# Kernel optimization log

Measured on AMD Instinct MI355X. Metric: run time of the kernel, lower is better.

## Reference

```python
import jax, jax.numpy as jnp
import numpy as np

B, T, C = 2, 2048, 1024
H = 4 * C           # MLP hidden (4*n_embd)
E_DYN = 7           # num_experts - static_experts
TOP_K = 2           # num_experts_per_tok
MOE_LOSS_COEF = 0.01


def setup_inputs() -> dict:
    key = jax.random.key(0)
    ks = jax.random.split(key, 6)
    s = 0.02
    x = jax.random.normal(ks[0], (B, T, C), dtype=jnp.float32)
    gate_w = jax.random.normal(ks[1], (C, E_DYN), dtype=jnp.float32) * s
    w1 = jax.random.normal(ks[2], (E_DYN, C, H), dtype=jnp.float32) * s   # dynamic experts c_fc
    w2 = jax.random.normal(ks[3], (E_DYN, H, C), dtype=jnp.float32) * s   # dynamic experts c_proj
    w1s = jax.random.normal(ks[4], (C, H), dtype=jnp.float32) * s         # static expert c_fc
    w2s = jax.random.normal(ks[5], (H, C), dtype=jnp.float32) * s         # static expert c_proj
    return {"x": x, "gate_w": gate_w, "w1": w1, "w2": w2, "w1s": w1s, "w2s": w2s}


def reference(x, gate_w, w1, w2, w1s, w2s):
    b, t, c = x.shape
    xf = x.reshape(-1, c)                                   # [N, C]
    n = xf.shape[0]

    # static expert (always applied)
    y_static = jax.nn.gelu(xf @ w1s, approximate=False) @ w2s  # [N, C]

    # gating: top-k + softmax over selected scores
    scores = xf @ gate_w                                    # [N, E]
    topk_scores, topk_idx = jax.lax.top_k(scores, TOP_K)    # [N, K]
    topk_w = jax.nn.softmax(topk_scores, axis=-1)           # [N, K]

    # dense dispatch weights [N, E] (top_k indices are distinct -> set is safe)
    probs = jnp.zeros((n, E_DYN), dtype=x.dtype)
    probs = probs.at[jnp.arange(n)[:, None], topk_idx].set(topk_w)

    # all-expert MLP then weighted combine (same math as masked per-expert dispatch)
    h = jax.nn.gelu(jnp.einsum('nc,ech->enh', xf, w1), approximate=False)  # [E, N, H]
    y_all = jnp.einsum('enh,ehc->enc', h, w2)               # [E, N, C]
    y_dyn = jnp.einsum('ne,enc->nc', probs, y_all)          # [N, C]

    y = (y_dyn + y_static).reshape(b, t, c)

    # variance_penalty auxiliary loss
    expert_usage = probs.mean(axis=0)                       # [E]
    variance = jnp.mean((expert_usage - expert_usage.mean()) ** 2)
    aux = MOE_LOSS_COEF * variance
    return y, aux
```

## Files before the change

kernel.cpp:

```cpp
#include <hip/hip_runtime.h>
#include <hip/hip_bf16.h>
#include <math.h>

#define N_TOK 4096
#define C_DIM 1024
#define H_DIM 4096
#define NEXP 7
#define NGRP 8
#define HCAP 13184

typedef __attribute__((ext_vector_type(8))) short short8;
typedef __attribute__((ext_vector_type(4))) float floatx4;

static const size_t OFF_COUNTS = 0;
static const size_t OFF_CURSOR = 64;
static const size_t OFF_BASE   = 128;
static const size_t OFF_PCOUNT = 192;
static const size_t OFF_CNT8   = 256;
static const size_t OFF_USAGE  = 320;
static const size_t OFF_TOPKI  = 4096;
static const size_t OFF_TOPKW  = OFF_TOPKI + 8192ull * 4;
static const size_t OFF_ETOK   = OFF_TOPKW + 8192ull * 4;
static const size_t OFF_EWT    = OFF_ETOK + (size_t)HCAP * 4;
static const size_t OFF_EIDX   = OFF_EWT + (size_t)HCAP * 4;
static const size_t OFF_XB     = 262144;
static const size_t OFF_W1T    = OFF_XB + (size_t)N_TOK * C_DIM * 2;
static const size_t OFF_W2T    = OFF_W1T + (size_t)NGRP * H_DIM * C_DIM * 2;
static const size_t OFF_H      = OFF_W2T + (size_t)NGRP * C_DIM * H_DIM * 2;

static __device__ __forceinline__ unsigned short f2bf(float f) {
    __hip_bfloat16 b = __float2bfloat16(f);
    return *reinterpret_cast<unsigned short*>(&b);
}
static __device__ __forceinline__ float bf2f(unsigned short u) {
    unsigned int v = ((unsigned int)u) << 16;
    return __builtin_bit_cast(float, v);
}

static __device__ __forceinline__ float gelu_f(float v) {
    float z = v * 0.70710678118654752f;
    float az = fabsf(z);
    float t = 1.0f / (1.0f + 0.3275911f * az);
    float poly = t * (0.254829592f + t * (-0.284496736f + t * (1.421413741f +
                 t * (-1.453152027f + t * 1.061405429f))));
    float erf_abs = 1.0f - poly * __expf(-az * az);
    float erf_v = (z < 0.f) ? -erf_abs : erf_abs;
    return 0.5f * v * (1.0f + erf_v);
}

static __device__ __forceinline__ void gll16(const void* g, void* l) {
    __builtin_amdgcn_global_load_lds((const __attribute__((address_space(1))) void*)g,
                                     (__attribute__((address_space(3))) void*)l, 16, 0, 0);
}

static __device__ __forceinline__ void barf() {
    __builtin_amdgcn_s_barrier();
    asm volatile("" ::: "memory");
}
#define LGKM0 asm volatile("s_waitcnt lgkmcnt(0)" ::: "memory")
#define VMC6  asm volatile("s_waitcnt vmcnt(6)" ::: "memory")
#define VMC0  asm volatile("s_waitcnt vmcnt(0)" ::: "memory")
#define PRIO1 __builtin_amdgcn_s_setprio(1)
#define PRIO0 __builtin_amdgcn_s_setprio(0)

__global__ void init_small_kernel(int* counts, int* cursor, float* usage) {
    int i = threadIdx.x;
    if (i < 8) { counts[i] = 0; cursor[i] = 0; usage[i] = 0.f; }
}

__global__ __launch_bounds__(256) void transpose_cvt_kernel(
    const float* __restrict__ w1, const float* __restrict__ w1s,
    const float* __restrict__ w2, const float* __restrict__ w2s,
    __hip_bfloat16* __restrict__ w1t, __hip_bfloat16* __restrict__ w2t)
{
    int bid = blockIdx.x;
    int fam = bid >> 13;
    int r = bid & 8191;
    int e = r >> 10;
    int t_ = r & 1023;
    int R, S, s0, r0;
    const float* src; unsigned short* d;
    if (fam == 0) {
        R = C_DIM; S = H_DIM;
        src = (e < NEXP) ? (w1 + (size_t)e * R * S) : w1s;
        d = (unsigned short*)(w1t) + (size_t)e * R * S;
        s0 = (t_ & 63) * 64; r0 = (t_ >> 6) * 64;
    } else {
        R = H_DIM; S = C_DIM;
        src = (e < NEXP) ? (w2 + (size_t)e * R * S) : w2s;
        d = (unsigned short*)(w2t) + (size_t)e * R * S;
        s0 = (t_ & 15) * 64; r0 = (t_ >> 4) * 64;
    }
    __shared__ float t[64][65];
    int lx = (threadIdx.x & 15) * 4, ty = threadIdx.x >> 4;
#pragma unroll
    for (int i = 0; i < 4; i++) {
        int rr = ty + i * 16;
        float4 v = *(const float4*)(src + (size_t)(r0 + rr) * S + s0 + lx);
        t[rr][lx] = v.x; t[rr][lx + 1] = v.y; t[rr][lx + 2] = v.z; t[rr][lx + 3] = v.w;
    }
    __syncthreads();
#pragma unroll
    for (int i = 0; i < 4; i++) {
        int ss = ty + i * 16;
        ushort4 o;
        o.x = f2bf(t[lx][ss]); o.y = f2bf(t[lx + 1][ss]);
        o.z = f2bf(t[lx + 2][ss]); o.w = f2bf(t[lx + 3][ss]);
        *(ushort4*)(d + (size_t)(s0 + ss) * R + r0 + lx) = o;
    }
}

__global__ __launch_bounds__(256) void gate_kernel(
    const float* __restrict__ x, const float* __restrict__ gw,
    unsigned short* __restrict__ xb,
    int* __restrict__ topki, float* __restrict__ topkw,
    int* counts, float* usage)
{
    int wid = threadIdx.x >> 6, lane = threadIdx.x & 63;
    int t = blockIdx.x * 4 + wid;
    float s[NEXP];
#pragma unroll
    for (int e = 0; e < NEXP; e++) s[e] = 0.f;
#pragma unroll
    for (int it = 0; it < 4; ++it) {
        int c = it * 256 + lane * 4;
        float4 xv = *(const float4*)(x + (size_t)t * C_DIM + c);
        ushort4 o;
        o.x = f2bf(xv.x); o.y = f2bf(xv.y); o.z = f2bf(xv.z); o.w = f2bf(xv.w);
        *(ushort4*)(xb + (size_t)t * C_DIM + c) = o;
        const float* g0 = gw + (size_t)c * NEXP;
#pragma unroll
        for (int e = 0; e < NEXP; e++) s[e] += xv.x * g0[e];
#pragma unroll
        for (int e = 0; e < NEXP; e++) s[e] += xv.y * g0[NEXP + e];
#pragma unroll
        for (int e = 0; e < NEXP; e++) s[e] += xv.z * g0[2 * NEXP + e];
#pragma unroll
        for (int e = 0; e < NEXP; e++) s[e] += xv.w * g0[3 * NEXP + e];
    }
#pragma unroll
    for (int e = 0; e < NEXP; e++)
        for (int off = 32; off > 0; off >>= 1) s[e] += __shfl_xor(s[e], off);
    if (lane == 0) {
        int e0 = 0;
        for (int e = 1; e < NEXP; e++) if (s[e] > s[e0]) e0 = e;
        int e1 = -1;
        for (int e = 0; e < NEXP; e++) {
            if (e == e0) continue;
            if (e1 < 0 || s[e] > s[e1]) e1 = e;
        }
        float w0 = 1.f / (1.f + expf(s[e1] - s[e0]));
        float w1 = 1.f - w0;
        topki[t * 2] = e0; topki[t * 2 + 1] = e1;
        topkw[t * 2] = w0; topkw[t * 2 + 1] = w1;
        atomicAdd(&counts[e0], 1); atomicAdd(&counts[e1], 1);
        atomicAdd(&usage[e0], w0); atomicAdd(&usage[e1], w1);
    }
}

__global__ __launch_bounds__(256) void prefix_kernel(
    const int* counts, const float* usage,
    int* base, int* pcount, int* cnt8,
    int* etok, float* ewt, float* y, int aux_index)
{
    __shared__ int sb[NGRP], sc[NGRP], sp[NGRP];
    if (threadIdx.x == 0) {
        int run = 0;
        for (int g = 0; g < NEXP; g++) {
            int c = counts[g];
            int p = (c + 127) & ~127;
            base[g] = run; pcount[g] = p; cnt8[g] = c;
            sb[g] = run; sc[g] = c; sp[g] = p;
            run += p;
        }
        base[NEXP] = run; pcount[NEXP] = N_TOK; cnt8[NEXP] = N_TOK;
        sb[NEXP] = run; sc[NEXP] = N_TOK; sp[NEXP] = N_TOK;
        float u[NEXP]; float mean = 0.f;
        for (int e = 0; e < NEXP; e++) { u[e] = usage[e] / (float)N_TOK; mean += u[e]; }
        mean /= (float)NEXP;
        float var = 0.f;
        for (int e = 0; e < NEXP; e++) { float dd = u[e] - mean; var += dd * dd; }
        var /= (float)NEXP;
        y[aux_index] = 0.01f * var;
    }
    __syncthreads();
    for (int i = threadIdx.x; i < N_TOK; i += 256) {
        etok[sb[NEXP] + i] = i; ewt[sb[NEXP] + i] = 1.0f;
    }
    for (int g = 0; g < NEXP; g++) {
        for (int i = sc[g] + (int)threadIdx.x; i < sp[g]; i += 256) {
            etok[sb[g] + i] = 0; ewt[sb[g] + i] = 0.f;
        }
    }
}

__global__ void scatter_kernel(const int* __restrict__ topki, const float* __restrict__ topkw,
                               const int* __restrict__ base, int* cursor,
                               int* __restrict__ etok, float* __restrict__ ewt,
                               int* __restrict__ eidx)
{
    int i = blockIdx.x * 256 + threadIdx.x;
    int t = i >> 1;
    int e = topki[i];
    float w = topkw[i];
    int pos = atomicAdd(&cursor[e], 1);
    int idx = base[e] + pos;
    etok[idx] = t; ewt[idx] = w;
    eidx[i] = idx;
}


static __device__ __forceinline__ void mfma16(const short8 (&a)[8], const short8 (&b)[4],
                                              floatx4 (&acc)[8][4], int mo, int no) {
#pragma unroll
    for (int i = 0; i < 4; i++)
#pragma unroll
        for (int j = 0; j < 2; j++)
#pragma unroll
            for (int kk = 0; kk < 2; kk++)
                acc[mo + i][no + j] = __builtin_amdgcn_mfma_f32_16x16x32_bf16(
                    a[i * 2 + kk], b[j * 2 + kk], acc[mo + i][no + j], 0, 0, 0);
}
static __device__ __forceinline__ void rdA(short8 (&d)[8], const char* b, int sw0, int sw1) {
#pragma unroll
    for (int i = 0; i < 4; i++) {
        d[i * 2]     = *(const short8*)(b + i * 2048 + sw0);
        d[i * 2 + 1] = *(const short8*)(b + i * 2048 + sw1);
    }
}
static __device__ __forceinline__ void rdB(short8 (&d)[4], const char* b, int sw0, int sw1) {
#pragma unroll
    for (int j = 0; j < 2; j++) {
        d[j * 2]     = *(const short8*)(b + j * 2048 + sw0);
        d[j * 2 + 1] = *(const short8*)(b + j * 2048 + sw1);
    }
}

static __device__ __forceinline__ void gemm_core(char* lds, int NKT,
    const char* pA0, const char* pA1, const char* pA2, const char* pA3,
    const char* pB0, const char* pB1, const char* pB2, const char* pB3,
    floatx4 (&acc)[8][4])
{
    int tid = threadIdx.x, lane = tid & 63, w = tid >> 6;
    int wm = w >> 2, wn = w & 3, l16 = lane & 15, quad = lane >> 4;
    int sw0 = ((quad ^ (l16 & 7)) << 4);
    int sw1 = (((4 + quad) ^ (l16 & 7)) << 4);
    int aoff = (wm * 64 + l16) * 128;
    int boff = (wn * 32 + l16) * 128;
    int wb = w * 1024;
    short8 aM0[8], aM1[8], bN0[4], bN1[4];

#define SA_(h, doff, ko) do { \
    gll16(((h) ? pA1 : pA0) + (ko), lds + (doff) + (h) * 16384 + wb); \
    gll16(((h) ? pA3 : pA2) + (ko), lds + (doff) + (h) * 16384 + 8192 + wb); } while (0)
#define SB_(nh, doff, ko) do { \
    gll16(((nh) ? pB1 : pB0) + (ko), lds + 65536 + (doff) + (nh) * 16384 + wb); \
    gll16(((nh) ? pB3 : pB2) + (ko), lds + 65536 + (doff) + (nh) * 16384 + 8192 + wb); } while (0)

    SA_(0, 0, 0); SA_(1, 0, 0); SB_(0, 0, 0); SB_(1, 0, 0);
    SA_(0, 32768, 128); SA_(1, 32768, 128); SB_(0, 32768, 128);
    VMC6;
    barf();

#pragma unroll 1
    for (int T = 0; T < NKT - 2; ++T) {
        int curo = (T & 1) << 15;
        int nxto = curo ^ 32768;
        rdB(bN0, lds + 65536 + curo + boff, sw0, sw1);
        rdA(aM0, lds + curo + aoff, sw0, sw1);
        SB_(1, nxto, 128);
        barf();
        PRIO1; mfma16(aM0, bN0, acc, 0, 0); PRIO0;
        LGKM0; barf();
        rdA(aM1, lds + curo + 16384 + aoff, sw0, sw1);
        SA_(0, curo, 256);
        barf();
        PRIO1; mfma16(aM1, bN0, acc, 4, 0); PRIO0;
        LGKM0; barf();
        rdB(bN1, lds + 65536 + curo + 16384 + boff, sw0, sw1);
        SA_(1, curo, 256);
        barf();
        PRIO1; mfma16(aM0, bN1, acc, 0, 2); PRIO0;
        LGKM0; barf();
        SB_(0, curo, 256);
        barf();
        PRIO1; mfma16(aM1, bN1, acc, 4, 2); PRIO0;
        VMC6;
        barf();
        pA0 += 128; pA1 += 128; pA2 += 128; pA3 += 128;
        pB0 += 128; pB1 += 128; pB2 += 128; pB3 += 128;
    }
    {
        int curo = ((NKT - 2) & 1) << 15;
        int nxto = curo ^ 32768;
        rdB(bN0, lds + 65536 + curo + boff, sw0, sw1);
        rdA(aM0, lds + curo + aoff, sw0, sw1);
        SB_(1, nxto, 128);
        barf();
        PRIO1; mfma16(aM0, bN0, acc, 0, 0); PRIO0;
        LGKM0; barf();
        rdA(aM1, lds + curo + 16384 + aoff, sw0, sw1);
        barf();
        PRIO1; mfma16(aM1, bN0, acc, 4, 0); PRIO0;
        LGKM0; barf();
        rdB(bN1, lds + 65536 + curo + 16384 + boff, sw0, sw1);
        barf();
        PRIO1; mfma16(aM0, bN1, acc, 0, 2); PRIO0;
        LGKM0; barf();
        PRIO1; mfma16(aM1, bN1, acc, 4, 2); PRIO0;
        VMC0;
        barf();
        int lasto = nxto;
        rdB(bN0, lds + 65536 + lasto + boff, sw0, sw1);
        rdA(aM0, lds + lasto + aoff, sw0, sw1);
        rdA(aM1, lds + lasto + 16384 + aoff, sw0, sw1);
        rdB(bN1, lds + 65536 + lasto + 16384 + boff, sw0, sw1);
        mfma16(aM0, bN0, acc, 0, 0);
        mfma16(aM1, bN0, acc, 4, 0);
        mfma16(aM0, bN1, acc, 0, 2);
        mfma16(aM1, bN1, acc, 4, 2);
    }
#undef SA_
#undef SB_
}

__global__ __launch_bounds__(512, 2) void gemm1_kernel(
    const __hip_bfloat16* __restrict__ xb,
    const __hip_bfloat16* __restrict__ w1t,
    __hip_bfloat16* __restrict__ h,
    const int* __restrict__ etok,
    const int* __restrict__ base,
    const int* __restrict__ pcount)
{
    int id = blockIdx.x;
    int xcd = id & 7, rest = id >> 3;
    int ct = rest & 15, s = rest >> 4;
    int g = s & 7;
    int mt = ((xcd - g) & 7) + 8 * (s >> 3);
    int psz = pcount[g];
    if (mt * 256 >= psz) return;
    int eb = base[g];

    __shared__ __align__(16) char lds[131072];

    int tid = threadIdx.x, lane = tid & 63, w = tid >> 6;
    int u0 = 8 * w + (lane >> 3);
    int v  = (u0 & 31) + ((u0 >> 5) << 6);
    int ssw = ((lane & 7) ^ (lane >> 3)) * 16;

    int t0 = etok[eb + mt * 256 + u0];
    int t1 = etok[eb + mt * 256 + 64 + u0];
    int t2 = etok[eb + mt * 256 + 128 + u0];
    int t3 = etok[eb + mt * 256 + 192 + u0];
    const char* pA0 = (const char*)(xb + (size_t)t0 * C_DIM) + ssw;
    const char* pA1 = (const char*)(xb + (size_t)t1 * C_DIM) + ssw;
    const char* pA2 = (const char*)(xb + (size_t)t2 * C_DIM) + ssw;
    const char* pA3 = (const char*)(xb + (size_t)t3 * C_DIM) + ssw;
    const char* pB0 = (const char*)(w1t + ((size_t)g * H_DIM + ct * 256 + v) * C_DIM) + ssw;
    const char* pB1 = (const char*)(w1t + ((size_t)g * H_DIM + ct * 256 + v + 32) * C_DIM) + ssw;
    const char* pB2 = (const char*)(w1t + ((size_t)g * H_DIM + ct * 256 + v + 128) * C_DIM) + ssw;
    const char* pB3 = (const char*)(w1t + ((size_t)g * H_DIM + ct * 256 + v + 160) * C_DIM) + ssw;

    floatx4 acc[8][4] = {};
    gemm_core(lds, C_DIM / 64, pA0, pA1, pA2, pA3, pB0, pB1, pB2, pB3, acc);

    int wm = w >> 2, wn = w & 3, l16 = lane & 15, quad = lane >> 4;
#pragma unroll
    for (int i = 0; i < 8; i++) {
        int lr0 = mt * 256 + wm * 128 + i * 16 + quad * 4;
#pragma unroll
        for (int reg = 0; reg < 4; reg++) {
            int lr = lr0 + reg;
            if (lr < psz) {
                size_t hrow = (size_t)(eb + lr) * H_DIM;
#pragma unroll
                for (int j = 0; j < 4; j++) {
                    int cc = ct * 256 + wn * 64 + j * 16 + l16;
                    h[hrow + cc] = __float2bfloat16(gelu_f(acc[i][j][reg]));
                }
            }
        }
    }
}

__global__ __launch_bounds__(512, 2) void gemm2_kernel(
    const __hip_bfloat16* __restrict__ h,
    const __hip_bfloat16* __restrict__ w2t,
    unsigned short* __restrict__ yp,
    const int* __restrict__ base,
    const int* __restrict__ pcount)
{
    int id = blockIdx.x;
    int xcd = id & 7, rest = id >> 3;
    int ct = rest & 3, s = rest >> 2;
    int g = s & 7;
    int mt = ((xcd - g) & 7) + 8 * (s >> 3);
    int psz = pcount[g];
    if (mt * 256 >= psz) return;
    int eb = base[g];

    __shared__ __align__(16) char lds[131072];

    int tid = threadIdx.x, lane = tid & 63, w = tid >> 6;
    int u0 = 8 * w + (lane >> 3);
    int v  = (u0 & 31) + ((u0 >> 5) << 6);
    int ssw = ((lane & 7) ^ (lane >> 3)) * 16;

    const char* pA0 = (const char*)(h + (size_t)(eb + mt * 256 + u0) * H_DIM) + ssw;
    const char* pA1 = (const char*)(h + (size_t)(eb + mt * 256 + 64 + u0) * H_DIM) + ssw;
    const char* pA2 = (const char*)(h + (size_t)(eb + mt * 256 + 128 + u0) * H_DIM) + ssw;
    const char* pA3 = (const char*)(h + (size_t)(eb + mt * 256 + 192 + u0) * H_DIM) + ssw;
    const char* pB0 = (const char*)(w2t + ((size_t)g * C_DIM + ct * 256 + v) * H_DIM) + ssw;
    const char* pB1 = (const char*)(w2t + ((size_t)g * C_DIM + ct * 256 + v + 32) * H_DIM) + ssw;
    const char* pB2 = (const char*)(w2t + ((size_t)g * C_DIM + ct * 256 + v + 128) * H_DIM) + ssw;
    const char* pB3 = (const char*)(w2t + ((size_t)g * C_DIM + ct * 256 + v + 160) * H_DIM) + ssw;

    floatx4 acc[8][4] = {};
    gemm_core(lds, H_DIM / 64, pA0, pA1, pA2, pA3, pB0, pB1, pB2, pB3, acc);

    int wm = w >> 2, wn = w & 3, l16 = lane & 15, quad = lane >> 4;
#pragma unroll
    for (int i = 0; i < 8; i++) {
        int lr0 = mt * 256 + wm * 128 + i * 16 + quad * 4;
#pragma unroll
        for (int reg = 0; reg < 4; reg++) {
            int lr = lr0 + reg;
            if (lr < psz) {
                size_t yrow = (size_t)(eb + lr) * C_DIM;
#pragma unroll
                for (int j = 0; j < 4; j++) {
                    int cc = ct * 256 + wn * 64 + j * 16 + l16;
                    yp[yrow + cc] = f2bf(acc[i][j][reg]);
                }
            }
        }
    }
}

__global__ __launch_bounds__(256) void combine_kernel(
    const unsigned short* __restrict__ yp,
    const int* __restrict__ eidx,
    const float* __restrict__ topkw,
    const int* __restrict__ base,
    float* __restrict__ y)
{
    int t = blockIdx.x;
    int i0 = eidx[t * 2], i1 = eidx[t * 2 + 1];
    float w0 = topkw[t * 2], w1 = topkw[t * 2 + 1];
    int is = base[NEXP] + t;
    int c = threadIdx.x * 4;
    ushort4 a = *(const ushort4*)(yp + (size_t)i0 * C_DIM + c);
    ushort4 b = *(const ushort4*)(yp + (size_t)i1 * C_DIM + c);
    ushort4 s = *(const ushort4*)(yp + (size_t)is * C_DIM + c);
    float4 o;
    o.x = w0 * bf2f(a.x) + w1 * bf2f(b.x) + bf2f(s.x);
    o.y = w0 * bf2f(a.y) + w1 * bf2f(b.y) + bf2f(s.y);
    o.z = w0 * bf2f(a.z) + w1 * bf2f(b.z) + bf2f(s.z);
    o.w = w0 * bf2f(a.w) + w1 * bf2f(b.w) + bf2f(s.w);
    *(float4*)(y + (size_t)t * C_DIM + c) = o;
}

extern "C" void kernel_launch(void* const* d_in, const int* in_sizes, int n_in,
                              void* d_out, int out_size, void* d_ws, size_t ws_size,
                              hipStream_t stream) {
    const float* x      = (const float*)d_in[0];
    const float* gate_w = (const float*)d_in[1];
    const float* w1     = (const float*)d_in[2];
    const float* w2     = (const float*)d_in[3];
    const float* w1s    = (const float*)d_in[4];
    const float* w2s    = (const float*)d_in[5];
    float* y = (float*)d_out;
    char* ws = (char*)d_ws;

    int*   counts = (int*)(ws + OFF_COUNTS);
    int*   cursor = (int*)(ws + OFF_CURSOR);
    int*   base   = (int*)(ws + OFF_BASE);
    int*   pcount = (int*)(ws + OFF_PCOUNT);
    int*   cnt8   = (int*)(ws + OFF_CNT8);
    float* usage  = (float*)(ws + OFF_USAGE);
    int*   topki  = (int*)(ws + OFF_TOPKI);
    float* topkw  = (float*)(ws + OFF_TOPKW);
    int*   etok   = (int*)(ws + OFF_ETOK);
    float* ewt    = (float*)(ws + OFF_EWT);
    int*   eidx   = (int*)(ws + OFF_EIDX);
    unsigned short* xb_u = (unsigned short*)(ws + OFF_XB);
    __hip_bfloat16* xb  = (__hip_bfloat16*)(ws + OFF_XB);
    __hip_bfloat16* w1t = (__hip_bfloat16*)(ws + OFF_W1T);
    __hip_bfloat16* w2t = (__hip_bfloat16*)(ws + OFF_W2T);
    __hip_bfloat16* hbuf = (__hip_bfloat16*)(ws + OFF_H);
    unsigned short* yp  = (unsigned short*)(ws + OFF_W1T);

    init_small_kernel<<<1, 64, 0, stream>>>(counts, cursor, usage);

    transpose_cvt_kernel<<<16384, 256, 0, stream>>>(w1, w1s, w2, w2s, w1t, w2t);

    gate_kernel<<<N_TOK / 4, 256, 0, stream>>>(x, gate_w, xb_u, topki, topkw, counts, usage);
    prefix_kernel<<<1, 256, 0, stream>>>(counts, usage, base, pcount, cnt8, etok, ewt, y, N_TOK * C_DIM);
    scatter_kernel<<<(N_TOK * 2) / 256, 256, 0, stream>>>(topki, topkw, base, cursor, etok, ewt, eidx);

    gemm1_kernel<<<4096, 512, 0, stream>>>(xb, w1t, hbuf, etok, base, pcount);
    gemm2_kernel<<<1024, 512, 0, stream>>>(hbuf, w2t, yp, base, pcount);
    combine_kernel<<<N_TOK, 256, 0, stream>>>(yp, eidx, topkw, base, y);
}
```

Baseline: 712.2 us.

## Restructure GEMM core pipeline to prefetch LDS fragments ahead of MFMAs

Reworks the shared GEMM main loop so LDS fragment reads for the next sub-tile are issued before the current MFMA batch, dropping the explicit lgkmcnt(0) waits. The loop is unrolled by two with compile-time buffer offsets, and K-tile counts and B strides become template parameters so the four B pointers collapse into one base plus constant offsets, freeing registers. The MFMA loop order is changed to iterate k outermost, and the occupancy hint of 2 blocks per CU is removed from launch_bounds. Overlapping LDS reads with MFMAs needs more live fragment registers and relies on the compiler inserting correct waits.

```diff
diff --git a/kernel.cpp b/kernel.cpp
--- a/kernel.cpp
+++ b/kernel.cpp
@@ -57,8 +57,7 @@
     __builtin_amdgcn_s_barrier();
     asm volatile("" ::: "memory");
 }
-#define LGKM0 asm volatile("s_waitcnt lgkmcnt(0)" ::: "memory")
-#define VMC6  asm volatile("s_waitcnt vmcnt(6)" ::: "memory")
+#define VMC2  asm volatile("s_waitcnt vmcnt(2)" ::: "memory")
 #define VMC0  asm volatile("s_waitcnt vmcnt(0)" ::: "memory")
 #define PRIO1 __builtin_amdgcn_s_setprio(1)
 #define PRIO0 __builtin_amdgcn_s_setprio(0)
@@ -213,11 +212,11 @@
 static __device__ __forceinline__ void mfma16(const short8 (&a)[8], const short8 (&b)[4],
                                               floatx4 (&acc)[8][4], int mo, int no) {
 #pragma unroll
-    for (int i = 0; i < 4; i++)
-#pragma unroll
-        for (int j = 0; j < 2; j++)
-#pragma unroll
-            for (int kk = 0; kk < 2; kk++)
+    for (int kk = 0; kk < 2; kk++)
+#pragma unroll
+        for (int i = 0; i < 4; i++)
+#pragma unroll
+            for (int j = 0; j < 2; j++)
                 acc[mo + i][no + j] = __builtin_amdgcn_mfma_f32_16x16x32_bf16(
                     a[i * 2 + kk], b[j * 2 + kk], acc[mo + i][no + j], 0, 0, 0);
 }
@@ -236,10 +235,10 @@
     }
 }
 
-static __device__ __forceinline__ void gemm_core(char* lds, int NKT,
+template <int NKT, size_t KB>
+static __device__ __forceinline__ void gemm_core(char* lds,
     const char* pA0, const char* pA1, const char* pA2, const char* pA3,
-    const char* pB0, const char* pB1, const char* pB2, const char* pB3,
-    floatx4 (&acc)[8][4])
+    const char* pB0, floatx4 (&acc)[8][4])
 {
     int tid = threadIdx.x, lane = tid & 63, w = tid >> 6;
     int wm = w >> 2, wn = w & 3, l16 = lane & 15, quad = lane >> 4;
@@ -254,68 +253,66 @@
     gll16(((h) ? pA1 : pA0) + (ko), lds + (doff) + (h) * 16384 + wb); \
     gll16(((h) ? pA3 : pA2) + (ko), lds + (doff) + (h) * 16384 + 8192 + wb); } while (0)
 #define SB_(nh, doff, ko) do { \
-    gll16(((nh) ? pB1 : pB0) + (ko), lds + 65536 + (doff) + (nh) * 16384 + wb); \
-    gll16(((nh) ? pB3 : pB2) + (ko), lds + 65536 + (doff) + (nh) * 16384 + 8192 + wb); } while (0)
+    gll16(pB0 + ((nh) ? 32 * KB : 0) + (ko), lds + 65536 + (doff) + (nh) * 16384 + wb); \
+    gll16(pB0 + ((nh) ? 160 * KB : 128 * KB) + (ko), lds + 65536 + (doff) + (nh) * 16384 + 8192 + wb); } while (0)
 
     SA_(0, 0, 0); SA_(1, 0, 0); SB_(0, 0, 0); SB_(1, 0, 0);
-    SA_(0, 32768, 128); SA_(1, 32768, 128); SB_(0, 32768, 128);
-    VMC6;
+    SA_(0, 32768, 128);
+    VMC2; barf();
+    SA_(1, 32768, 128);
+    rdB(bN0, lds + 65536 + boff, sw0, sw1);
+    SB_(0, 32768, 128);
+    rdA(aM0, lds + aoff, sw0, sw1);
     barf();
 
-#pragma unroll 1
-    for (int T = 0; T < NKT - 2; ++T) {
-        int curo = (T & 1) << 15;
-        int nxto = curo ^ 32768;
-        rdB(bN0, lds + 65536 + curo + boff, sw0, sw1);
-        rdA(aM0, lds + curo + aoff, sw0, sw1);
-        SB_(1, nxto, 128);
+#define STEP(CUR, NXT) do { \
+         \
+        rdA(aM1, lds + (CUR) + 16384 + aoff, sw0, sw1); \
+        SB_(1, (NXT), 128); \
+        PRIO1; mfma16(aM0, bN0, acc, 0, 0); PRIO0; \
+        barf(); \
+         \
+        rdB(bN1, lds + 65536 + (CUR) + 16384 + boff, sw0, sw1); \
+        SA_(0, (CUR), 256); \
+        PRIO1; mfma16(aM1, bN0, acc, 4, 0); PRIO0; \
+        VMC2; barf(); \
+         \
+        rdB(bN0, lds + 65536 + (NXT) + boff, sw0, sw1); \
+        SA_(1, (CUR), 256); \
+        PRIO1; mfma16(aM0, bN1, acc, 0, 2); PRIO0; \
+        barf(); \
+         \
+        rdA(aM0, lds + (NXT) + aoff, sw0, sw1); \
+        SB_(0, (CUR), 256); \
+        PRIO1; mfma16(aM1, bN1, acc, 4, 2); PRIO0; \
+        barf(); \
+        pA0 += 128; pA1 += 128; pA2 += 128; pA3 += 128; pB0 += 128; \
+    } while (0)
+
+    for (int T = 0; T < NKT - 2; T += 2) {
+        STEP(0, 32768);
+        STEP(32768, 0);
+    }
+#undef STEP
+
+    {
+        const int CUR = ((NKT - 2) & 1) << 15, NXT = CUR ^ 32768;
+        rdA(aM1, lds + CUR + 16384 + aoff, sw0, sw1);
+        SB_(1, NXT, 128);
+        PRIO1; mfma16(aM0, bN0, acc, 0, 0); PRIO0;
         barf();
-        PRIO1; mfma16(aM0, bN0, acc, 0, 0); PRIO0;
-        LGKM0; barf();
-        rdA(aM1, lds + curo + 16384 + aoff, sw0, sw1);
-        SA_(0, curo, 256);
+        rdB(bN1, lds + 65536 + CUR + 16384 + boff, sw0, sw1);
+        PRIO1; mfma16(aM1, bN0, acc, 4, 0); PRIO0;
+        VMC0; barf();
+        rdB(bN0, lds + 65536 + NXT + boff, sw0, sw1);
+        PRIO1; mfma16(aM0, bN1, acc, 0, 2); PRIO0;
         barf();
-        PRIO1; mfma16(aM1, bN0, acc, 4, 0); PRIO0;
-        LGKM0; barf();
-        rdB(bN1, lds + 65536 + curo + 16384 + boff, sw0, sw1);
-        SA_(1, curo, 256);
+        rdA(aM0, lds + NXT + aoff, sw0, sw1);
+        PRIO1; mfma16(aM1, bN1, acc, 4, 2); PRIO0;
         barf();
-        PRIO1; mfma16(aM0, bN1, acc, 0, 2); PRIO0;
-        LGKM0; barf();
-        SB_(0, curo, 256);
-        barf();
-        PRIO1; mfma16(aM1, bN1, acc, 4, 2); PRIO0;
-        VMC6;
-        barf();
-        pA0 += 128; pA1 += 128; pA2 += 128; pA3 += 128;
-        pB0 += 128; pB1 += 128; pB2 += 128; pB3 += 128;
-    }
-    {
-        int curo = ((NKT - 2) & 1) << 15;
-        int nxto = curo ^ 32768;
-        rdB(bN0, lds + 65536 + curo + boff, sw0, sw1);
-        rdA(aM0, lds + curo + aoff, sw0, sw1);
-        SB_(1, nxto, 128);
-        barf();
-        PRIO1; mfma16(aM0, bN0, acc, 0, 0); PRIO0;
-        LGKM0; barf();
-        rdA(aM1, lds + curo + 16384 + aoff, sw0, sw1);
-        barf();
-        PRIO1; mfma16(aM1, bN0, acc, 4, 0); PRIO0;
-        LGKM0; barf();
-        rdB(bN1, lds + 65536 + curo + 16384 + boff, sw0, sw1);
-        barf();
-        PRIO1; mfma16(aM0, bN1, acc, 0, 2); PRIO0;
-        LGKM0; barf();
-        PRIO1; mfma16(aM1, bN1, acc, 4, 2); PRIO0;
-        VMC0;
-        barf();
-        int lasto = nxto;
-        rdB(bN0, lds + 65536 + lasto + boff, sw0, sw1);
-        rdA(aM0, lds + lasto + aoff, sw0, sw1);
-        rdA(aM1, lds + lasto + 16384 + aoff, sw0, sw1);
-        rdB(bN1, lds + 65536 + lasto + 16384 + boff, sw0, sw1);
+        rdA(aM1, lds + NXT + 16384 + aoff, sw0, sw1);
         mfma16(aM0, bN0, acc, 0, 0);
+        rdB(bN1, lds + 65536 + NXT + 16384 + boff, sw0, sw1);
         mfma16(aM1, bN0, acc, 4, 0);
         mfma16(aM0, bN1, acc, 0, 2);
         mfma16(aM1, bN1, acc, 4, 2);
@@ -324,7 +321,7 @@
 #undef SB_
 }
 
-__global__ __launch_bounds__(512, 2) void gemm1_kernel(
+__global__ __launch_bounds__(512) void gemm1_kernel(
     const __hip_bfloat16* __restrict__ xb,
     const __hip_bfloat16* __restrict__ w1t,
     __hip_bfloat16* __restrict__ h,
@@ -357,12 +354,9 @@
     const char* pA2 = (const char*)(xb + (size_t)t2 * C_DIM) + ssw;
     const char* pA3 = (const char*)(xb + (size_t)t3 * C_DIM) + ssw;
     const char* pB0 = (const char*)(w1t + ((size_t)g * H_DIM + ct * 256 + v) * C_DIM) + ssw;
-    const char* pB1 = (const char*)(w1t + ((size_t)g * H_DIM + ct * 256 + v + 32) * C_DIM) + ssw;
-    const char* pB2 = (const char*)(w1t + ((size_t)g * H_DIM + ct * 256 + v + 128) * C_DIM) + ssw;
-    const char* pB3 = (const char*)(w1t + ((size_t)g * H_DIM + ct * 256 + v + 160) * C_DIM) + ssw;
 
     floatx4 acc[8][4] = {};
-    gemm_core(lds, C_DIM / 64, pA0, pA1, pA2, pA3, pB0, pB1, pB2, pB3, acc);
+    gemm_core<C_DIM / 64, 2048>(lds, pA0, pA1, pA2, pA3, pB0, acc);
 
     int wm = w >> 2, wn = w & 3, l16 = lane & 15, quad = lane >> 4;
 #pragma unroll
@@ -383,7 +377,7 @@
     }
 }
 
-__global__ __launch_bounds__(512, 2) void gemm2_kernel(
+__global__ __launch_bounds__(512) void gemm2_kernel(
     const __hip_bfloat16* __restrict__ h,
     const __hip_bfloat16* __restrict__ w2t,
     unsigned short* __restrict__ yp,
@@ -411,12 +405,9 @@
     const char* pA2 = (const char*)(h + (size_t)(eb + mt * 256 + 128 + u0) * H_DIM) + ssw;
     const char* pA3 = (const char*)(h + (size_t)(eb + mt * 256 + 192 + u0) * H_DIM) + ssw;
     const char* pB0 = (const char*)(w2t + ((size_t)g * C_DIM + ct * 256 + v) * H_DIM) + ssw;
-    const char* pB1 = (const char*)(w2t + ((size_t)g * C_DIM + ct * 256 + v + 32) * H_DIM) + ssw;
-    const char* pB2 = (const char*)(w2t + ((size_t)g * C_DIM + ct * 256 + v + 128) * H_DIM) + ssw;
-    const char* pB3 = (const char*)(w2t + ((size_t)g * C_DIM + ct * 256 + v + 160) * H_DIM) + ssw;
 
     floatx4 acc[8][4] = {};
-    gemm_core(lds, H_DIM / 64, pA0, pA1, pA2, pA3, pB0, pB1, pB2, pB3, acc);
+    gemm_core<H_DIM / 64, 8192>(lds, pA0, pA1, pA2, pA3, pB0, acc);
 
     int wm = w >> 2, wn = w & 3, l16 = lane & 15, quad = lane >> 4;
 #pragma unroll
```

Result: slower. 895.6 us (+25.7%).
